# Performance work log

Measured on AMD Instinct MI355X. Metric: run time of the kernel, lower is better.

The kernel has to match this reference:

```python
import jax, jax.numpy as jnp
import numpy as np

EMBED_DIM = 512
BLOCK = 511
N_HEAD = 8
N_GLOBAL = 4
N_LOCAL = 2
N_MIX = 2
RECEP = 4
T = 2 * BLOCK + 2  # [task, clip, BLOCK upper, BLOCK lower]
HD = EMBED_DIM // N_HEAD
NEG = -1e9


def _build_masks():
    bs = BLOCK
    temporal = np.concatenate([np.zeros(2), np.arange(bs) * 2 + 1, np.arange(bs) * 2 + 2])
    seq = temporal[None, :] <= temporal[:, None]  # causal over interleaved temporal order
    tq = np.concatenate([np.arange(bs) * 2 + 1 - 2 * RECEP + 1] * 2)
    tk = np.concatenate([np.arange(bs) * 2 + 1] * 2)
    de = tk[None, :] < tq[:, None]  # keys too far in the past for the sliding window
    local = seq.copy()
    local[2:, 2:] = local[2:, 2:] & ~de
    return jnp.asarray(local), jnp.asarray(seq)


LOCAL_MASK, GLOBAL_MASK = _build_masks()  # (T, T) bool, True = visible


def _linear_params(key, fan_in, fan_out):
    k1, k2 = jax.random.split(key)
    s = 1.0 / np.sqrt(fan_in)
    W = jax.random.uniform(k1, (fan_out, fan_in), minval=-s, maxval=s, dtype=jnp.float32)
    b = jax.random.uniform(k2, (fan_out,), minval=-s, maxval=s, dtype=jnp.float32)
    return W, b


def setup_inputs() -> dict:
    key = jax.random.key(0)
    ks = jax.random.split(key, 10)
    B = 4
    x = jax.random.normal(ks[0], (B, T, EMBED_DIM), dtype=jnp.float32)
    cond_mask = jnp.ones((B, T), dtype=jnp.float32)
    Wq, bq = _linear_params(ks[1], EMBED_DIM, EMBED_DIM)
    Wk, bk = _linear_params(ks[2], EMBED_DIM, EMBED_DIM)
    Wv, bv = _linear_params(ks[3], EMBED_DIM, EMBED_DIM)
    Wqml, bqml = _linear_params(ks[4], EMBED_DIM, HD * N_MIX)
    Wkml, bkml = _linear_params(ks[5], EMBED_DIM, HD * N_MIX)
    Wp, bp = _linear_params(ks[6], EMBED_DIM, EMBED_DIM)
    mix_w = jax.random.normal(ks[7], (N_MIX, 2), dtype=jnp.float32) * 0.5  # Conv2d(2*nm, nm, groups=nm, 1x1)
    bias_clip = jnp.full((1, N_HEAD, 1), 0.5, dtype=jnp.float32)
    bias_clip_ml = jnp.full((1, N_MIX, 1), 0.5, dtype=jnp.float32)
    return dict(x=x, cond_mask=cond_mask, Wq=Wq, bq=bq, Wk=Wk, bk=bk, Wv=Wv, bv=bv,
                Wqml=Wqml, bqml=bqml, Wkml=Wkml, bkml=bkml, mix_w=mix_w, Wp=Wp, bp=bp,
                bias_clip=bias_clip, bias_clip_ml=bias_clip_ml)


def reference(x, cond_mask, Wq, bq, Wk, bk, Wv, bv, Wqml, bqml, Wkml, bkml, mix_w, Wp, bp, bias_clip, bias_clip_ml):
    B, Tx, C = x.shape

    def heads(W, b, nh):
        return (x @ W.T + b).reshape(B, Tx, nh, HD).transpose(0, 2, 1, 3)  # (B, nh, T, hd)

    q = heads(Wq, bq, N_HEAD)
    k = heads(Wk, bk, N_HEAD)
    v = heads(Wv, bv, N_HEAD)
    qml = heads(Wqml, bqml, N_MIX)
    kml = heads(Wkml, bkml, N_MIX)

    scale = 1.0 / np.sqrt(HD)
    # main attention: heads [0:N_LOCAL] local-masked, rest global (causal) masked
    att = jnp.einsum('bhqd,bhkd->bhqk', q, k) * scale
    att = att.at[:, :, :, 1].add(bias_clip)  # learned bias on the CLIP-token key column
    head_mask = jnp.concatenate([
        jnp.broadcast_to(LOCAL_MASK, (N_LOCAL, Tx, Tx)),
        jnp.broadcast_to(GLOBAL_MASK, (N_MIX + N_GLOBAL, Tx, Tx))], axis=0)
    att = jax.nn.softmax(jnp.where(head_mask[None], att, NEG), axis=-1)

    # extra local-masked score maps for the mix heads
    aml = jnp.einsum('bhqd,bhkd->bhqk', qml, kml) * scale
    aml = aml.at[:, :, :, 1].add(bias_clip_ml)
    aml = jax.nn.softmax(jnp.where(LOCAL_MASK[None, None], aml, NEG), axis=-1)

    # grouped 1x1 conv: per mix head, blend (global, local) attention maps
    mix_in = jnp.stack([att[:, N_LOCAL:N_LOCAL + N_MIX], aml], axis=2)  # (B, nm, 2, T, T)
    mix_out = jnp.einsum('ho,bhoqk->bhqk', mix_w, mix_in)

    att_f = jnp.concatenate([att[:, :N_LOCAL], mix_out, att[:, N_LOCAL + N_MIX:]], axis=1)
    y = jnp.einsum('bhqk,bhkd->bhqd', att_f, v)
    y = y.transpose(0, 2, 1, 3).reshape(B, Tx, C)
    return y @ Wp.T + bp
```

## Files before the change

### kernel.cpp

```cpp
#include <hip/hip_runtime.h>

typedef unsigned short u16;
typedef __attribute__((ext_vector_type(8))) __bf16 bf16x8;
typedef __attribute__((ext_vector_type(4))) float f32x4;
typedef __attribute__((ext_vector_type(8))) short short8;
typedef __attribute__((ext_vector_type(4))) u16 us4;

#define T_SEQ 1024
#define PW 1280

__device__ __forceinline__ u16 f2bf(float f) {
  unsigned u = __float_as_uint(f);
  u += 0x7fff + ((u >> 16) & 1);
  return (u16)(u >> 16);
}

__constant__ u16 GLOB_M[16] = {0x0101,0x0303,0x0707,0x0F0F,0x1F1F,0x3F3F,0x7F7F,0xFFFF,
                               0xFFFF,0x0307,0x070F,0x0F1F,0x1F3F,0x3F7F,0x7FFF,0xFFFF};
__constant__ u16 LOC_M[16]  = {0x0101,0x0303,0x0607,0x0C0D,0x1819,0x3031,0x6061,0xC0C1,
                               0x8183,0x0307,0x060F,0x0C1D,0x1839,0x3071,0x60E1,0xC1C1};

__global__ void prep_all(const float4* __restrict__ x, u16* __restrict__ xb,
                         const float* __restrict__ Wq, const float* __restrict__ Wk,
                         const float* __restrict__ Wv, const float* __restrict__ Wqml,
                         const float* __restrict__ Wkml, const float* __restrict__ Wp,
                         const float* __restrict__ bq, const float* __restrict__ bk,
                         const float* __restrict__ bv, const float* __restrict__ bqml,
                         const float* __restrict__ bkml,
                         u16* __restrict__ Wcat, u16* __restrict__ Wpx, float* __restrict__ bcat) {
  if (blockIdx.x < 2048) {
    int i = blockIdx.x * 256 + threadIdx.x;
    float4 v = x[i];
    us4 o = { f2bf(v.x), f2bf(v.y), f2bf(v.z), f2bf(v.w) };
    *(us4*)&xb[i * 4] = o;
    return;
  }
  int idx = (blockIdx.x - 2048) * 256 + threadIdx.x;
  const int NW = 1792 * 512;
  if (idx < NW) {
    int row = idx >> 9;
    float v;
    if (row < 512)       v = Wq[idx];
    else if (row < 1024) v = Wk[idx - 512 * 512];
    else if (row < 1536) v = Wv[idx - 1024 * 512];
    else if (row < 1664) v = Wqml[idx - 1536 * 512];
    else                 v = Wkml[idx - 1664 * 512];
    Wcat[idx] = f2bf(v);
    return;
  }
  int i2 = idx - NW;
  if (i2 < 512 * 640) {
    int n = i2 / 640, k2 = i2 - n * 640;
    float v = (k2 < 512) ? Wp[n * 512 + k2] : Wp[n * 512 + k2 - 384];
    Wpx[i2] = f2bf(v);
    return;
  }
  int i3 = i2 - 512 * 640;
  if (i3 < 1792) {
    float v;
    if (i3 < 512)       v = bq[i3];
    else if (i3 < 1024) v = bk[i3 - 512];
    else if (i3 < 1536) v = bv[i3 - 1024];
    else if (i3 < 1664) v = bqml[i3 - 1536];
    else                v = bkml[i3 - 1664];
    bcat[i3] = v;
  }
}


__device__ __forceinline__ void stage64(const u16* __restrict__ G, int row0,
                                        u16* lbase, int t, int w) {
#pragma unroll
  for (int j = 0; j < 2; ++j) {
    const u16* gp = &G[(size_t)(row0 + j * 64 + (t >> 2)) * 512 + (t & 3) * 8];
    u16* lp = lbase + j * 2048 + w * 512;
    __builtin_amdgcn_global_load_lds((const __attribute__((address_space(1))) unsigned*)gp,
                                     (__attribute__((address_space(3))) unsigned*)lp,
                                     16, 0, 0);
  }
}

__global__ __launch_bounds__(256) void gemm_qkv(
    const u16* __restrict__ A, const u16* __restrict__ Bw,
    const float* __restrict__ bias, u16* __restrict__ Pout, u16* __restrict__ Vtb) {
  __shared__ u16 As[2][4096];
  __shared__ u16 Bs[2][4096];
  const int tid = threadIdx.x;
  const int lane = tid & 63, w = tid >> 6;
  const int g = lane >> 4, c = lane & 15;
  const int n0 = blockIdx.x * 128, m0 = blockIdx.y * 128;
  const int wm = (w >> 1) * 64, wn = (w & 1) * 64;

  f32x4 acc[4][4] = {};
  stage64(&A[(size_t)m0 * 512], 0, As[0], tid, w);
  stage64(&Bw[(size_t)n0 * 512], 0, Bs[0], tid, w);
  __syncthreads();
  for (int ks = 0; ks < 16; ++ks) {
    int cur = ks & 1;
    if (ks + 1 < 16) {
      stage64(&A[(size_t)m0 * 512 + (ks + 1) * 32], 0, As[cur ^ 1], tid, w);
      stage64(&Bw[(size_t)n0 * 512 + (ks + 1) * 32], 0, Bs[cur ^ 1], tid, w);
    }
    bf16x8 av[4], bv[4];
#pragma unroll
    for (int f = 0; f < 4; ++f) {
      av[f] = *(const bf16x8*)&As[cur][(wm + f * 16 + c) * 32 + g * 8];
      bv[f] = *(const bf16x8*)&Bs[cur][(wn + f * 16 + c) * 32 + g * 8];
    }
#pragma unroll
    for (int fm = 0; fm < 4; ++fm)
#pragma unroll
      for (int fn = 0; fn < 4; ++fn)
        acc[fm][fn] = __builtin_amdgcn_mfma_f32_16x16x32_bf16(av[fm], bv[fn], acc[fm][fn], 0, 0, 0);
    __syncthreads();
  }

  const bool isV = (n0 >= 1024 && n0 < 1536);
#pragma unroll
  for (int fm = 0; fm < 4; ++fm)
#pragma unroll
    for (int fn = 0; fn < 4; ++fn) {
      int row = m0 + wm + fm * 16 + g * 4;
      int col = n0 + wn + fn * 16 + c;
      float bb = bias[col];
      if (isV) {
        int d = col - 1024;
        int bidx = row >> 10, t = row & 1023;
        us4 pack = { f2bf(acc[fm][fn][0] + bb), f2bf(acc[fm][fn][1] + bb),
                     f2bf(acc[fm][fn][2] + bb), f2bf(acc[fm][fn][3] + bb) };
        *(us4*)&Vtb[((size_t)bidx * 512 + d) * 1024 + t] = pack;
      } else {
        int pcol = (col < 1024) ? col : col - 512;
#pragma unroll
        for (int r = 0; r < 4; ++r)
          Pout[(size_t)(row + r) * PW + pcol] = f2bf(acc[fm][fn][r] + bb);
      }
    }
}

template<bool OUT_BF16>
__global__ __launch_bounds__(256) void gemm_bt(
    const u16* __restrict__ A, int lda,
    const u16* __restrict__ Bw, int ldb,
    const float* __restrict__ bias,
    void* __restrict__ Cout, int ldc, int K) {
  __shared__ u16 As[64][40];
  __shared__ u16 Bs[64][40];
  const int tid = threadIdx.x;
  const int lane = tid & 63, w = tid >> 6;
  const int g = lane >> 4, c = lane & 15;
  const int m0 = blockIdx.y * 64, n0 = blockIdx.x * 64;
  const int wr = (w >> 1) * 32, wc = (w & 1) * 32;
  const int arow = tid >> 2, acol = (tid & 3) * 8;

  f32x4 acc[2][2] = {};
  for (int k0 = 0; k0 < K; k0 += 32) {
    short8 av = *(const short8*)&A[(size_t)(m0 + arow) * lda + k0 + acol];
    short8 bv = *(const short8*)&Bw[(size_t)(n0 + arow) * ldb + k0 + acol];
    *(short8*)&As[arow][acol] = av;
    *(short8*)&Bs[arow][acol] = bv;
    __syncthreads();
    bf16x8 a0 = *(const bf16x8*)&As[wr + c][g * 8];
    bf16x8 a1 = *(const bf16x8*)&As[wr + 16 + c][g * 8];
    bf16x8 b0 = *(const bf16x8*)&Bs[wc + c][g * 8];
    bf16x8 b1 = *(const bf16x8*)&Bs[wc + 16 + c][g * 8];
    acc[0][0] = __builtin_amdgcn_mfma_f32_16x16x32_bf16(a0, b0, acc[0][0], 0, 0, 0);
    acc[0][1] = __builtin_amdgcn_mfma_f32_16x16x32_bf16(a0, b1, acc[0][1], 0, 0, 0);
    acc[1][0] = __builtin_amdgcn_mfma_f32_16x16x32_bf16(a1, b0, acc[1][0], 0, 0, 0);
    acc[1][1] = __builtin_amdgcn_mfma_f32_16x16x32_bf16(a1, b1, acc[1][1], 0, 0, 0);
    __syncthreads();
  }
  for (int fm = 0; fm < 2; ++fm)
    for (int fn = 0; fn < 2; ++fn)
      for (int r = 0; r < 4; ++r) {
        int row = m0 + wr + fm * 16 + g * 4 + r;
        int col = n0 + wc + fn * 16 + c;
        float v = acc[fm][fn][r] + bias[col];
        if constexpr (OUT_BF16) ((u16*)Cout)[(size_t)row * ldc + col] = f2bf(v);
        else                    ((float*)Cout)[(size_t)row * ldc + col] = v;
      }
}

__global__ __launch_bounds__(256) void attn_k(
    const u16* __restrict__ P, const u16* __restrict__ Vtb, u16* __restrict__ Y,
    float* __restrict__ Part,
    const float* __restrict__ mix_w, const float* __restrict__ bias_clip,
    const float* __restrict__ bias_clip_ml) {
  __shared__ u16 Ks[64][72];
  __shared__ u16 Vs[64][72];
  __shared__ u16 Ps[4][16][72];
  const int tid = threadIdx.x, lane = tid & 63, w = tid >> 6;
  const int g = lane >> 4, c = lane & 15;
  const int qt = blockIdx.x, u = blockIdx.y, b = blockIdx.z;

  int qcol, kcol, vsel, outcol = 0, hp = 0, sp = 0;
  bool localMask = false, split = false;
  float kbias, wgt = 1.0f;
  if (u < 2) {
    qcol = u * 64; kcol = 512 + u * 64; vsel = u; outcol = u * 64;
    localMask = true; kbias = bias_clip[u];
  } else if (u < 14) {
    int h = 2 + ((u - 2) >> 1); sp = (u - 2) & 1; split = true; hp = h - 2;
    qcol = h * 64; kcol = 512 + h * 64; vsel = h; kbias = bias_clip[h];
  } else {
    int mh = u - 14;
    qcol = 1024 + mh * 64; kcol = 1152 + mh * 64; vsel = 2 + mh; outcol = 512 + mh * 64;
    localMask = true; kbias = bias_clip_ml[mh]; wgt = mix_w[mh * 2 + 1];
  }
  unsigned mask = localMask ? (unsigned)LOC_M[qt] : (unsigned)GLOB_M[qt];
  if (split) mask &= sp ? 0xAAAAu : 0x5555u;

  const size_t baseP = (size_t)b * T_SEQ * PW;
  const u16* __restrict__ Vbase = Vtb + ((size_t)b * 512 + vsel * 64) * 1024;
  const int r0 = qt * 64 + w * 16;
  const int srow = tid >> 2, scol = (tid & 3) * 16;

  int upmax[4], lomax[4], wminr[4];
#pragma unroll
  for (int r = 0; r < 4; ++r) {
    int row = r0 + g * 4 + r;
    int tqr = (row < 2) ? 0 : ((row < 513) ? 2 * row - 3 : 2 * row - 1024);
    upmax[r] = (tqr - 1) >> 1;
    lomax[r] = (tqr - 2) >> 1;
    wminr[r] = (localMask && row >= 2) ? ((row < 513 ? row - 2 : row - 513) - 3) : -1000000;
  }

  float m[4], l[4];
  f32x4 o[4] = {};
#pragma unroll
  for (int r = 0; r < 4; ++r) { m[r] = -1e8f; l[r] = 0.0f; }

  if (mask) {
    const int qrow = r0 + c;
    bf16x8 aq0 = *(const bf16x8*)&P[baseP + (size_t)qrow * PW + qcol + g * 8];
    bf16x8 aq1 = *(const bf16x8*)&P[baseP + (size_t)qrow * PW + qcol + 32 + g * 8];

    unsigned rem = mask;
    int kt = __ffs(rem) - 1; rem &= rem - 1;
    short8 ka, kb2, va, vb2;
    {
      const u16* kp = &P[baseP + (size_t)(kt * 64 + srow) * PW + kcol + scol];
      ka = *(const short8*)kp; kb2 = *(const short8*)(kp + 8);
      const u16* vp = &Vbase[(size_t)srow * 1024 + kt * 64 + scol];
      va = *(const short8*)vp; vb2 = *(const short8*)(vp + 8);
    }

    for (;;) {
      __syncthreads();
      *(short8*)&Ks[srow][scol] = ka;
      *(short8*)&Ks[srow][scol + 8] = kb2;
      *(short8*)&Vs[srow][scol] = va;
      *(short8*)&Vs[srow][scol + 8] = vb2;
      __syncthreads();

      int ktn = -1;
      if (rem) {
        ktn = __ffs(rem) - 1; rem &= rem - 1;
        const u16* kp = &P[baseP + (size_t)(ktn * 64 + srow) * PW + kcol + scol];
        ka = *(const short8*)kp; kb2 = *(const short8*)(kp + 8);
        const u16* vp = &Vbase[(size_t)srow * 1024 + ktn * 64 + scol];
        va = *(const short8*)vp; vb2 = *(const short8*)(vp + 8);
      }

      const int k0 = kt * 64;
      float s[4][4];
#pragma unroll
      for (int cb = 0; cb < 4; ++cb) {
        f32x4 accs = {};
        bf16x8 bk0 = *(const bf16x8*)&Ks[cb * 16 + c][g * 8];
        bf16x8 bk1 = *(const bf16x8*)&Ks[cb * 16 + c][32 + g * 8];
        accs = __builtin_amdgcn_mfma_f32_16x16x32_bf16(aq0, bk0, accs, 0, 0, 0);
        accs = __builtin_amdgcn_mfma_f32_16x16x32_bf16(aq1, bk1, accs, 0, 0, 0);
#pragma unroll
        for (int r = 0; r < 4; ++r) s[cb][r] = accs[r] * 0.125f;
      }
#pragma unroll
      for (int cb = 0; cb < 4; ++cb) {
        int colg = k0 + cb * 16 + c;
        bool tok = colg < 2;
        bool low = colg >= 513;
        int jk = colg - (low ? 513 : 2);
        float addb = (colg == 1) ? kbias : 0.0f;
#pragma unroll
        for (int r = 0; r < 4; ++r) {
          int bnd = low ? lomax[r] : upmax[r];
          bool vis = tok | ((jk <= bnd) & (jk >= wminr[r]));
          s[cb][r] = vis ? (s[cb][r] + addb) : -1e9f;
        }
      }
#pragma unroll
      for (int r = 0; r < 4; ++r) {
        float rmax = fmaxf(fmaxf(s[0][r], s[1][r]), fmaxf(s[2][r], s[3][r]));
        for (int off = 1; off < 16; off <<= 1)
          rmax = fmaxf(rmax, __shfl_xor(rmax, off));
        float mnew = fmaxf(m[r], rmax);
        float fr = __expf(m[r] - mnew);
        float psum = 0.0f;
#pragma unroll
        for (int cb = 0; cb < 4; ++cb) {
          float p = __expf(s[cb][r] - mnew);
          s[cb][r] = p;
          psum += p;
        }
        for (int off = 1; off < 16; off <<= 1)
          psum += __shfl_xor(psum, off);
        l[r] = l[r] * fr + psum;
        m[r] = mnew;
#pragma unroll
        for (int db = 0; db < 4; ++db) o[db][r] *= fr;
      }
#pragma unroll
      for (int cb = 0; cb < 4; ++cb)
#pragma unroll
        for (int r = 0; r < 4; ++r)
          Ps[w][g * 4 + r][cb * 16 + c] = f2bf(s[cb][r]);
      asm volatile("s_waitcnt lgkmcnt(0)" ::: "memory");
      __builtin_amdgcn_sched_barrier(0);
#pragma unroll
      for (int ks2 = 0; ks2 < 2; ++ks2) {
        bf16x8 ap = *(const bf16x8*)&Ps[w][c][ks2 * 32 + g * 8];
#pragma unroll
        for (int db = 0; db < 4; ++db) {
          bf16x8 bv = *(const bf16x8*)&Vs[db * 16 + c][ks2 * 32 + g * 8];
          o[db] = __builtin_amdgcn_mfma_f32_16x16x32_bf16(ap, bv, o[db], 0, 0, 0);
        }
      }
      if (ktn < 0) break;
      kt = ktn;
    }
  }

  if (split) {
    float* pb = Part + (size_t)((hp * 2 + sp) * 4 + b) * T_SEQ * 68;
#pragma unroll
    for (int r = 0; r < 4; ++r) {
      int row = r0 + g * 4 + r;
#pragma unroll
      for (int db = 0; db < 4; ++db)
        pb[(size_t)row * 68 + db * 16 + c] = o[db][r];
      if (c == 0) {
        pb[(size_t)row * 68 + 64] = m[r];
        pb[(size_t)row * 68 + 65] = l[r];
      }
    }
  } else {
    float wl[4];
#pragma unroll
    for (int r = 0; r < 4; ++r) wl[r] = wgt / l[r];
#pragma unroll
    for (int db = 0; db < 4; ++db)
#pragma unroll
      for (int r = 0; r < 4; ++r) {
        int row = r0 + g * 4 + r;
        int col = outcol + db * 16 + c;
        Y[((size_t)b * T_SEQ + row) * 640 + col] = f2bf(o[db][r] * wl[r]);
      }
  }
}

__global__ __launch_bounds__(256) void combine_k(
    const float* __restrict__ Part, u16* __restrict__ Y,
    const float* __restrict__ mix_w) {
  int idx = blockIdx.x * 256 + threadIdx.x;
  int q4 = idx & 15;
  int row = (idx >> 4) & 1023;
  int hb = idx >> 14;
  int hp = hb >> 2, b = hb & 3;
  const float* p1 = Part + ((size_t)((hp * 2 + 0) * 4 + b) * 1024 + row) * 68;
  const float* p2 = Part + ((size_t)((hp * 2 + 1) * 4 + b) * 1024 + row) * 68;
  float m1 = p1[64], l1 = p1[65];
  float m2 = p2[64], l2 = p2[65];
  float ms = fmaxf(m1, m2);
  float e1 = __expf(m1 - ms), e2 = __expf(m2 - ms);
  float wgt = (hp < 2) ? mix_w[hp * 2] : 1.0f;
  float inv = wgt / (l1 * e1 + l2 * e2);
  float4 o1 = *(const float4*)&p1[q4 * 4];
  float4 o2 = *(const float4*)&p2[q4 * 4];
  us4 pack = { f2bf((o1.x * e1 + o2.x * e2) * inv),
               f2bf((o1.y * e1 + o2.y * e2) * inv),
               f2bf((o1.z * e1 + o2.z * e2) * inv),
               f2bf((o1.w * e1 + o2.w * e2) * inv) };
  *(us4*)&Y[((size_t)b * 1024 + row) * 640 + (hp + 2) * 64 + q4 * 4] = pack;
}

extern "C" void kernel_launch(void* const* d_in, const int* in_sizes, int n_in,
                              void* d_out, int out_size, void* d_ws, size_t ws_size,
                              hipStream_t stream) {
  const float* x     = (const float*)d_in[0];
  const float* Wq    = (const float*)d_in[2];
  const float* bq    = (const float*)d_in[3];
  const float* Wk    = (const float*)d_in[4];
  const float* bk    = (const float*)d_in[5];
  const float* Wv    = (const float*)d_in[6];
  const float* bv    = (const float*)d_in[7];
  const float* Wqml  = (const float*)d_in[8];
  const float* bqml  = (const float*)d_in[9];
  const float* Wkml  = (const float*)d_in[10];
  const float* bkml  = (const float*)d_in[11];
  const float* mixw  = (const float*)d_in[12];
  const float* Wp    = (const float*)d_in[13];
  const float* bp    = (const float*)d_in[14];
  const float* bclip = (const float*)d_in[15];
  const float* bclipml = (const float*)d_in[16];

  u16* xb   = (u16*)d_ws;
  u16* Wcat = xb + 4096 * 512;
  u16* Wpx  = Wcat + 1792 * 512;
  u16* Ybuf = Wpx + 512 * 640;
  u16* Vtb  = Ybuf + 4096 * 640;
  u16* Pbuf = Vtb + 4 * 512 * 1024;
  float* bcat = (float*)(Pbuf + 4096 * 1280);
  float* Part = bcat + 2048;

  prep_all<<<6919, 256, 0, stream>>>((const float4*)x, xb, Wq, Wk, Wv, Wqml, Wkml, Wp,
                                     bq, bk, bv, bqml, bkml, Wcat, Wpx, bcat);
  gemm_qkv<<<dim3(14, 32), 256, 0, stream>>>(xb, Wcat, bcat, Pbuf, Vtb);
  attn_k<<<dim3(16, 16, 4), 256, 0, stream>>>(Pbuf, Vtb, Ybuf, Part, mixw, bclip, bclipml);
  combine_k<<<1536, 256, 0, stream>>>(Part, Ybuf, mixw);
  gemm_bt<false><<<dim3(8, 64), 256, 0, stream>>>(Ybuf, 640, Wpx, 640, bp,
                                                  (void*)d_out, 512, 640);
}
```

Before: 88.23 us.

## Swizzle LDS tiles with async loads, 4-way split global heads, bf16 partials

All three main kernels now stage tiles through global_load_lds into XOR-swizzled LDS layouts. The QKV GEMM moves to a 64-wide K step, the output projection becomes a 128x64-tile double-buffered GEMM, and attention double-buffers K/V through async LDS loads. The global heads are split four ways instead of two, which raises the attention grid from 16 to 28 y-blocks, and the partial outputs are stored as bf16 instead of f32. The combine step now merges four partials. These changes aim to remove LDS bank conflicts, register-staged copies and partial-buffer traffic, at the cost of more partial merges and reduced precision in the partials.

```diff
diff --git a/kernel.cpp b/kernel.cpp
--- a/kernel.cpp
+++ b/kernel.cpp
@@ -14,11 +14,35 @@
   u += 0x7fff + ((u >> 16) & 1);
   return (u16)(u >> 16);
 }
+__device__ __forceinline__ float bf2f(u16 v) {
+  return __uint_as_float((unsigned)v << 16);
+}
 
 __constant__ u16 GLOB_M[16] = {0x0101,0x0303,0x0707,0x0F0F,0x1F1F,0x3F3F,0x7F7F,0xFFFF,
                                0xFFFF,0x0307,0x070F,0x0F1F,0x1F3F,0x3F7F,0x7FFF,0xFFFF};
 __constant__ u16 LOC_M[16]  = {0x0101,0x0303,0x0607,0x0C0D,0x1819,0x3031,0x6061,0xC0C1,
                                0x8183,0x0307,0x060F,0x0C1D,0x1839,0x3071,0x60E1,0xC1C1};
+
+__device__ __forceinline__ void gll16(const u16* gp, u16* lp) {
+  __builtin_amdgcn_global_load_lds((const __attribute__((address_space(1))) unsigned*)gp,
+                                   (__attribute__((address_space(3))) unsigned*)lp, 16, 0, 0);
+}
+
+template<int NISS>
+__device__ __forceinline__ void stage_sw(u16* lds, const u16* __restrict__ g,
+                                         int ld, int tid) {
+  const int w = tid >> 6;
+#pragma unroll
+  for (int i = 0; i < NISS; ++i) {
+    int row = i * 32 + (tid >> 3);
+    int cswz = ((tid & 7) << 4) ^ ((row & 7) << 4);
+    gll16(g + (size_t)row * ld + (cswz >> 1), lds + i * 2048 + w * 512);
+  }
+}
+
+__device__ __forceinline__ bf16x8 rd_sw(const u16* lds, int row, int colbyte) {
+  return *(const bf16x8*)&lds[row * 64 + ((colbyte ^ ((row & 7) << 4)) >> 1)];
+}
 
 __global__ void prep_all(const float4* __restrict__ x, u16* __restrict__ xb,
                          const float* __restrict__ Wq, const float* __restrict__ Wk,
@@ -67,24 +91,11 @@
   }
 }
 
-
-__device__ __forceinline__ void stage64(const u16* __restrict__ G, int row0,
-                                        u16* lbase, int t, int w) {
-#pragma unroll
-  for (int j = 0; j < 2; ++j) {
-    const u16* gp = &G[(size_t)(row0 + j * 64 + (t >> 2)) * 512 + (t & 3) * 8];
-    u16* lp = lbase + j * 2048 + w * 512;
-    __builtin_amdgcn_global_load_lds((const __attribute__((address_space(1))) unsigned*)gp,
-                                     (__attribute__((address_space(3))) unsigned*)lp,
-                                     16, 0, 0);
-  }
-}
-
 __global__ __launch_bounds__(256) void gemm_qkv(
     const u16* __restrict__ A, const u16* __restrict__ Bw,
     const float* __restrict__ bias, u16* __restrict__ Pout, u16* __restrict__ Vtb) {
-  __shared__ u16 As[2][4096];
-  __shared__ u16 Bs[2][4096];
+  __shared__ u16 As[2][8192];
+  __shared__ u16 Bs[2][8192];
   const int tid = threadIdx.x;
   const int lane = tid & 63, w = tid >> 6;
   const int g = lane >> 4, c = lane & 15;
@@ -92,26 +103,29 @@
   const int wm = (w >> 1) * 64, wn = (w & 1) * 64;
 
   f32x4 acc[4][4] = {};
-  stage64(&A[(size_t)m0 * 512], 0, As[0], tid, w);
-  stage64(&Bw[(size_t)n0 * 512], 0, Bs[0], tid, w);
+  stage_sw<4>(As[0], A + (size_t)m0 * 512, 512, tid);
+  stage_sw<4>(Bs[0], Bw + (size_t)n0 * 512, 512, tid);
   __syncthreads();
-  for (int ks = 0; ks < 16; ++ks) {
+  for (int ks = 0; ks < 8; ++ks) {
     int cur = ks & 1;
-    if (ks + 1 < 16) {
-      stage64(&A[(size_t)m0 * 512 + (ks + 1) * 32], 0, As[cur ^ 1], tid, w);
-      stage64(&Bw[(size_t)n0 * 512 + (ks + 1) * 32], 0, Bs[cur ^ 1], tid, w);
-    }
-    bf16x8 av[4], bv[4];
-#pragma unroll
-    for (int f = 0; f < 4; ++f) {
-      av[f] = *(const bf16x8*)&As[cur][(wm + f * 16 + c) * 32 + g * 8];
-      bv[f] = *(const bf16x8*)&Bs[cur][(wn + f * 16 + c) * 32 + g * 8];
-    }
-#pragma unroll
-    for (int fm = 0; fm < 4; ++fm)
-#pragma unroll
-      for (int fn = 0; fn < 4; ++fn)
-        acc[fm][fn] = __builtin_amdgcn_mfma_f32_16x16x32_bf16(av[fm], bv[fn], acc[fm][fn], 0, 0, 0);
+    if (ks + 1 < 8) {
+      stage_sw<4>(As[cur ^ 1], A + (size_t)m0 * 512 + (ks + 1) * 64, 512, tid);
+      stage_sw<4>(Bs[cur ^ 1], Bw + (size_t)n0 * 512 + (ks + 1) * 64, 512, tid);
+    }
+#pragma unroll
+    for (int h = 0; h < 2; ++h) {
+      bf16x8 av[4], bv[4];
+#pragma unroll
+      for (int f = 0; f < 4; ++f) {
+        av[f] = rd_sw(As[cur], wm + f * 16 + c, h * 64 + g * 16);
+        bv[f] = rd_sw(Bs[cur], wn + f * 16 + c, h * 64 + g * 16);
+      }
+#pragma unroll
+      for (int fm = 0; fm < 4; ++fm)
+#pragma unroll
+        for (int fn = 0; fn < 4; ++fn)
+          acc[fm][fn] = __builtin_amdgcn_mfma_f32_16x16x32_bf16(av[fm], bv[fn], acc[fm][fn], 0, 0, 0);
+    }
     __syncthreads();
   }
 
@@ -138,82 +152,91 @@
     }
 }
 
-template<bool OUT_BF16>
-__global__ __launch_bounds__(256) void gemm_bt(
-    const u16* __restrict__ A, int lda,
-    const u16* __restrict__ Bw, int ldb,
-    const float* __restrict__ bias,
-    void* __restrict__ Cout, int ldc, int K) {
-  __shared__ u16 As[64][40];
-  __shared__ u16 Bs[64][40];
+__global__ __launch_bounds__(256) void gemm_out(
+    const u16* __restrict__ A, const u16* __restrict__ Bw,
+    const float* __restrict__ bias, float* __restrict__ Cout) {
+  __shared__ u16 As[2][8192];
+  __shared__ u16 Bs[2][4096];
   const int tid = threadIdx.x;
   const int lane = tid & 63, w = tid >> 6;
   const int g = lane >> 4, c = lane & 15;
-  const int m0 = blockIdx.y * 64, n0 = blockIdx.x * 64;
-  const int wr = (w >> 1) * 32, wc = (w & 1) * 32;
-  const int arow = tid >> 2, acol = (tid & 3) * 8;
-
-  f32x4 acc[2][2] = {};
-  for (int k0 = 0; k0 < K; k0 += 32) {
-    short8 av = *(const short8*)&A[(size_t)(m0 + arow) * lda + k0 + acol];
-    short8 bv = *(const short8*)&Bw[(size_t)(n0 + arow) * ldb + k0 + acol];
-    *(short8*)&As[arow][acol] = av;
-    *(short8*)&Bs[arow][acol] = bv;
+  const int n0 = blockIdx.x * 64, m0 = blockIdx.y * 128;
+  const int wm = (w >> 1) * 64, wn = (w & 1) * 32;
+
+  f32x4 acc[4][2] = {};
+  stage_sw<4>(As[0], A + (size_t)m0 * 640, 640, tid);
+  stage_sw<2>(Bs[0], Bw + (size_t)n0 * 640, 640, tid);
+  __syncthreads();
+  for (int ks = 0; ks < 10; ++ks) {
+    int cur = ks & 1;
+    if (ks + 1 < 10) {
+      stage_sw<4>(As[cur ^ 1], A + (size_t)m0 * 640 + (ks + 1) * 64, 640, tid);
+      stage_sw<2>(Bs[cur ^ 1], Bw + (size_t)n0 * 640 + (ks + 1) * 64, 640, tid);
+    }
+#pragma unroll
+    for (int h = 0; h < 2; ++h) {
+      bf16x8 av[4], bv[2];
+#pragma unroll
+      for (int f = 0; f < 4; ++f)
+        av[f] = rd_sw(As[cur], wm + f * 16 + c, h * 64 + g * 16);
+#pragma unroll
+      for (int f = 0; f < 2; ++f)
+        bv[f] = rd_sw(Bs[cur], wn + f * 16 + c, h * 64 + g * 16);
+#pragma unroll
+      for (int fm = 0; fm < 4; ++fm)
+#pragma unroll
+        for (int fn = 0; fn < 2; ++fn)
+          acc[fm][fn] = __builtin_amdgcn_mfma_f32_16x16x32_bf16(av[fm], bv[fn], acc[fm][fn], 0, 0, 0);
+    }
     __syncthreads();
-    bf16x8 a0 = *(const bf16x8*)&As[wr + c][g * 8];
-    bf16x8 a1 = *(const bf16x8*)&As[wr + 16 + c][g * 8];
-    bf16x8 b0 = *(const bf16x8*)&Bs[wc + c][g * 8];
-    bf16x8 b1 = *(const bf16x8*)&Bs[wc + 16 + c][g * 8];
-    acc[0][0] = __builtin_amdgcn_mfma_f32_16x16x32_bf16(a0, b0, acc[0][0], 0, 0, 0);
-    acc[0][1] = __builtin_amdgcn_mfma_f32_16x16x32_bf16(a0, b1, acc[0][1], 0, 0, 0);
-    acc[1][0] = __builtin_amdgcn_mfma_f32_16x16x32_bf16(a1, b0, acc[1][0], 0, 0, 0);
-    acc[1][1] = __builtin_amdgcn_mfma_f32_16x16x32_bf16(a1, b1, acc[1][1], 0, 0, 0);
-    __syncthreads();
-  }
-  for (int fm = 0; fm < 2; ++fm)
+  }
+#pragma unroll
+  for (int fm = 0; fm < 4; ++fm)
+#pragma unroll
     for (int fn = 0; fn < 2; ++fn)
+#pragma unroll
       for (int r = 0; r < 4; ++r) {
-        int row = m0 + wr + fm * 16 + g * 4 + r;
-        int col = n0 + wc + fn * 16 + c;
-        float v = acc[fm][fn][r] + bias[col];
-        if constexpr (OUT_BF16) ((u16*)Cout)[(size_t)row * ldc + col] = f2bf(v);
-        else                    ((float*)Cout)[(size_t)row * ldc + col] = v;
+        int row = m0 + wm + fm * 16 + g * 4 + r;
+        int col = n0 + wn + fn * 16 + c;
+        Cout[(size_t)row * 512 + col] = acc[fm][fn][r] + bias[col];
       }
 }
 
 __global__ __launch_bounds__(256) void attn_k(
     const u16* __restrict__ P, const u16* __restrict__ Vtb, u16* __restrict__ Y,
-    float* __restrict__ Part,
+    u16* __restrict__ Part_o, float* __restrict__ Part_ml,
     const float* __restrict__ mix_w, const float* __restrict__ bias_clip,
     const float* __restrict__ bias_clip_ml) {
-  __shared__ u16 Ks[64][72];
-  __shared__ u16 Vs[64][72];
+  __shared__ u16 Ks[2][4096];
+  __shared__ u16 Vs[2][4096];
   __shared__ u16 Ps[4][16][72];
   const int tid = threadIdx.x, lane = tid & 63, w = tid >> 6;
   const int g = lane >> 4, c = lane & 15;
   const int qt = blockIdx.x, u = blockIdx.y, b = blockIdx.z;
 
-  int qcol, kcol, vsel, outcol = 0, hp = 0, sp = 0;
-  bool localMask = false, split = false;
+  int qcol, kcol, vsel, outcol = 0, slot = -1;
+  bool localMask = false;
   float kbias, wgt = 1.0f;
-  if (u < 2) {
-    qcol = u * 64; kcol = 512 + u * 64; vsel = u; outcol = u * 64;
-    localMask = true; kbias = bias_clip[u];
-  } else if (u < 14) {
-    int h = 2 + ((u - 2) >> 1); sp = (u - 2) & 1; split = true; hp = h - 2;
+  unsigned mask;
+  if (u < 24) {
+    int h = 2 + (u >> 2), sp = u & 3; slot = u;
     qcol = h * 64; kcol = 512 + h * 64; vsel = h; kbias = bias_clip[h];
+    mask = (unsigned)GLOB_M[qt] & (0x1111u << sp);
+  } else if (u < 26) {
+    int h = u - 24;
+    qcol = h * 64; kcol = 512 + h * 64; vsel = h; outcol = h * 64;
+    localMask = true; kbias = bias_clip[h];
+    mask = LOC_M[qt];
   } else {
-    int mh = u - 14;
+    int mh = u - 26;
     qcol = 1024 + mh * 64; kcol = 1152 + mh * 64; vsel = 2 + mh; outcol = 512 + mh * 64;
     localMask = true; kbias = bias_clip_ml[mh]; wgt = mix_w[mh * 2 + 1];
-  }
-  unsigned mask = localMask ? (unsigned)LOC_M[qt] : (unsigned)GLOB_M[qt];
-  if (split) mask &= sp ? 0xAAAAu : 0x5555u;
-
+    mask = LOC_M[qt];
+  }
   const size_t baseP = (size_t)b * T_SEQ * PW;
+  const u16* __restrict__ Kbase = P + baseP + kcol;
   const u16* __restrict__ Vbase = Vtb + ((size_t)b * 512 + vsel * 64) * 1024;
   const int r0 = qt * 64 + w * 16;
-  const int srow = tid >> 2, scol = (tid & 3) * 16;
 
   int upmax[4], lomax[4], wminr[4];
 #pragma unroll
@@ -237,29 +260,17 @@
 
     unsigned rem = mask;
     int kt = __ffs(rem) - 1; rem &= rem - 1;
-    short8 ka, kb2, va, vb2;
-    {
-      const u16* kp = &P[baseP + (size_t)(kt * 64 + srow) * PW + kcol + scol];
-      ka = *(const short8*)kp; kb2 = *(const short8*)(kp + 8);
-      const u16* vp = &Vbase[(size_t)srow * 1024 + kt * 64 + scol];
-      va = *(const short8*)vp; vb2 = *(const short8*)(vp + 8);
-    }
+    stage_sw<2>(Ks[0], Kbase + (size_t)(kt * 64) * PW, PW, tid);
+    stage_sw<2>(Vs[0], Vbase + kt * 64, 1024, tid);
+    __syncthreads();
+    int cur = 0;
 
     for (;;) {
-      __syncthreads();
-      *(short8*)&Ks[srow][scol] = ka;
-      *(short8*)&Ks[srow][scol + 8] = kb2;
-      *(short8*)&Vs[srow][scol] = va;
-      *(short8*)&Vs[srow][scol + 8] = vb2;
-      __syncthreads();
-
       int ktn = -1;
       if (rem) {
         ktn = __ffs(rem) - 1; rem &= rem - 1;
-        const u16* kp = &P[baseP + (size_t)(ktn * 64 + srow) * PW + kcol + scol];
-        ka = *(const short8*)kp; kb2 = *(const short8*)(kp + 8);
-        const u16* vp = &Vbase[(size_t)srow * 1024 + ktn * 64 + scol];
-        va = *(const short8*)vp; vb2 = *(const short8*)(vp + 8);
+        stage_sw<2>(Ks[cur ^ 1], Kbase + (size_t)(ktn * 64) * PW, PW, tid);
+        stage_sw<2>(Vs[cur ^ 1], Vbase + ktn * 64, 1024, tid);
       }
 
       const int k0 = kt * 64;
@@ -267,8 +278,8 @@
 #pragma unroll
       for (int cb = 0; cb < 4; ++cb) {
         f32x4 accs = {};
-        bf16x8 bk0 = *(const bf16x8*)&Ks[cb * 16 + c][g * 8];
-        bf16x8 bk1 = *(const bf16x8*)&Ks[cb * 16 + c][32 + g * 8];
+        bf16x8 bk0 = rd_sw(Ks[cur], cb * 16 + c, g * 16);
+        bf16x8 bk1 = rd_sw(Ks[cur], cb * 16 + c, 64 + g * 16);
         accs = __builtin_amdgcn_mfma_f32_16x16x32_bf16(aq0, bk0, accs, 0, 0, 0);
         accs = __builtin_amdgcn_mfma_f32_16x16x32_bf16(aq1, bk1, accs, 0, 0, 0);
 #pragma unroll
@@ -321,26 +332,29 @@
         bf16x8 ap = *(const bf16x8*)&Ps[w][c][ks2 * 32 + g * 8];
 #pragma unroll
         for (int db = 0; db < 4; ++db) {
-          bf16x8 bv = *(const bf16x8*)&Vs[db * 16 + c][ks2 * 32 + g * 8];
+          bf16x8 bv = rd_sw(Vs[cur], db * 16 + c, ks2 * 64 + g * 16);
           o[db] = __builtin_amdgcn_mfma_f32_16x16x32_bf16(ap, bv, o[db], 0, 0, 0);
         }
       }
+
       if (ktn < 0) break;
-      kt = ktn;
-    }
-  }
-
-  if (split) {
-    float* pb = Part + (size_t)((hp * 2 + sp) * 4 + b) * T_SEQ * 68;
+      __syncthreads();
+      cur ^= 1; kt = ktn;
+    }
+  }
+
+  if (slot >= 0) {
+    u16* po = Part_o + ((size_t)(slot * 4 + b)) * T_SEQ * 64;
 #pragma unroll
     for (int r = 0; r < 4; ++r) {
       int row = r0 + g * 4 + r;
 #pragma unroll
       for (int db = 0; db < 4; ++db)
-        pb[(size_t)row * 68 + db * 16 + c] = o[db][r];
+        po[(size_t)row * 64 + db * 16 + c] = f2bf(o[db][r]);
       if (c == 0) {
-        pb[(size_t)row * 68 + 64] = m[r];
-        pb[(size_t)row * 68 + 65] = l[r];
+        size_t mlb = (((size_t)(slot * 4 + b)) * T_SEQ + row) * 2;
+        Part_ml[mlb] = m[r];
+        Part_ml[mlb + 1] = l[r];
       }
     }
   } else {
@@ -359,28 +373,36 @@
 }
 
 __global__ __launch_bounds__(256) void combine_k(
-    const float* __restrict__ Part, u16* __restrict__ Y,
-    const float* __restrict__ mix_w) {
+    const u16* __restrict__ Part_o, const float* __restrict__ Part_ml,
+    u16* __restrict__ Y, const float* __restrict__ mix_w) {
   int idx = blockIdx.x * 256 + threadIdx.x;
   int q4 = idx & 15;
   int row = (idx >> 4) & 1023;
-  int hb = idx >> 14;
-  int hp = hb >> 2, b = hb & 3;
-  const float* p1 = Part + ((size_t)((hp * 2 + 0) * 4 + b) * 1024 + row) * 68;
-  const float* p2 = Part + ((size_t)((hp * 2 + 1) * 4 + b) * 1024 + row) * 68;
-  float m1 = p1[64], l1 = p1[65];
-  float m2 = p2[64], l2 = p2[65];
-  float ms = fmaxf(m1, m2);
-  float e1 = __expf(m1 - ms), e2 = __expf(m2 - ms);
+  int bb = (idx >> 14) & 3;
+  int hp = idx >> 16;
+  float mv[4], lv[4];
+  float ms = -1e30f;
+#pragma unroll
+  for (int s = 0; s < 4; ++s) {
+    size_t base = (((size_t)(hp * 4 + s) * 4 + bb) * 1024 + row) * 2;
+    mv[s] = Part_ml[base];
+    lv[s] = Part_ml[base + 1];
+    ms = fmaxf(ms, mv[s]);
+  }
+  float denom = 0.0f, e[4];
+#pragma unroll
+  for (int s = 0; s < 4; ++s) { e[s] = __expf(mv[s] - ms); denom += lv[s] * e[s]; }
   float wgt = (hp < 2) ? mix_w[hp * 2] : 1.0f;
-  float inv = wgt / (l1 * e1 + l2 * e2);
-  float4 o1 = *(const float4*)&p1[q4 * 4];
-  float4 o2 = *(const float4*)&p2[q4 * 4];
-  us4 pack = { f2bf((o1.x * e1 + o2.x * e2) * inv),
-               f2bf((o1.y * e1 + o2.y * e2) * inv),
-               f2bf((o1.z * e1 + o2.z * e2) * inv),
-               f2bf((o1.w * e1 + o2.w * e2) * inv) };
-  *(us4*)&Y[((size_t)b * 1024 + row) * 640 + (hp + 2) * 64 + q4 * 4] = pack;
+  float inv = wgt / denom;
+  float out[4] = {0.f, 0.f, 0.f, 0.f};
+#pragma unroll
+  for (int s = 0; s < 4; ++s) {
+    us4 ov = *(const us4*)&Part_o[(((size_t)(hp * 4 + s) * 4 + bb) * 1024 + row) * 64 + q4 * 4];
+#pragma unroll
+    for (int j = 0; j < 4; ++j) out[j] += e[s] * bf2f(ov[j]);
+  }
+  us4 pk = { f2bf(out[0] * inv), f2bf(out[1] * inv), f2bf(out[2] * inv), f2bf(out[3] * inv) };
+  *(us4*)&Y[((size_t)bb * 1024 + row) * 640 + (hp + 2) * 64 + q4 * 4] = pk;
 }
 
 extern "C" void kernel_launch(void* const* d_in, const int* in_sizes, int n_in,
@@ -410,13 +432,14 @@
   u16* Vtb  = Ybuf + 4096 * 640;
   u16* Pbuf = Vtb + 4 * 512 * 1024;
   float* bcat = (float*)(Pbuf + 4096 * 1280);
-  float* Part = bcat + 2048;
+  u16* Part_o = (u16*)(bcat + 2048);
+  float* Part_ml = (float*)(Part_o + 24 * 4 * 1024 * 64);
 
   prep_all<<<6919, 256, 0, stream>>>((const float4*)x, xb, Wq, Wk, Wv, Wqml, Wkml, Wp,
                                      bq, bk, bv, bqml, bkml, Wcat, Wpx, bcat);
   gemm_qkv<<<dim3(14, 32), 256, 0, stream>>>(xb, Wcat, bcat, Pbuf, Vtb);
-  attn_k<<<dim3(16, 16, 4), 256, 0, stream>>>(Pbuf, Vtb, Ybuf, Part, mixw, bclip, bclipml);
-  combine_k<<<1536, 256, 0, stream>>>(Part, Ybuf, mixw);
-  gemm_bt<false><<<dim3(8, 64), 256, 0, stream>>>(Ybuf, 640, Wpx, 640, bp,
-                                                  (void*)d_out, 512, 640);
-}
+  attn_k<<<dim3(16, 28, 4), 256, 0, stream>>>(Pbuf, Vtb, Ybuf, Part_o, Part_ml,
+                                              mixw, bclip, bclipml);
+  combine_k<<<1536, 256, 0, stream>>>(Part_o, Part_ml, Ybuf, mixw);
+  gemm_out<<<dim3(8, 32), 256, 0, stream>>>(Ybuf, Wpx, bp, (float*)d_out);
+}
```

After: 83.66 us. 1.05x faster.
